# Kernel optimization log

Hardware: AMD Instinct MI355X
Metric: run time of the kernel (lower is better)

The kernel has to match this reference:

```python
import jax, jax.numpy as jnp
import numpy as np


def setup_inputs() -> dict:
    key = jax.random.key(0)
    k1, k2 = jax.random.split(key)
    B, C, H, W = 16, 128, 128, 128
    x = jax.random.normal(k1, (B, C, H, W), dtype=jnp.float32)
    # 1x1 conv weight, no bias: [out_channels, in_channels]
    w = jax.random.normal(k2, (C, C), dtype=jnp.float32) * (1.0 / np.sqrt(C))
    return {"x": x, "w": w}


def reference(x, w):
    # x: [B, C, H, W]; original computes y = x @ (x^T x) / (H*W) over flattened
    # spatial dim N = H*W, then a 1x1 conv. We reassociate exactly:
    #   x @ (x^T x) == (x x^T) @ x   (associativity of matmul)
    # avoiding the O(N^2) intermediate; math is identical.
    B, C, H, W = x.shape
    N = H * W
    xf = x.reshape(B, C, N)                              # [B, C, N]
    gram = jnp.einsum('bcn,bdn->bcd', xf, xf) / N        # [B, C, C] = (x x^T)/N
    y = jnp.einsum('bcd,bdn->bcn', gram, xf)             # [B, C, N]
    y = y.reshape(B, C, H, W)
    # 1x1 conv (bias=False) == per-pixel channel mixing
    out = jnp.einsum('oc,bchw->bohw', w, y)              # [B, C, H, W]
    return out
```

## Files before the change

kernel.cpp:

```cpp
#include <hip/hip_runtime.h>

typedef __attribute__((ext_vector_type(8))) short bf16x8;
typedef __attribute__((ext_vector_type(4))) float f32x4;
typedef __attribute__((ext_vector_type(4))) float f4v;
typedef __attribute__((ext_vector_type(4))) unsigned short u16x4;

#define NB 16
#define NC 128
#define NN 16384

__device__ __forceinline__ unsigned int f2bf_pack(float lo, float hi) {
  unsigned int ulo = __float_as_uint(lo);
  unsigned int uhi = __float_as_uint(hi);
  ulo = (ulo + 0x7FFFu + ((ulo >> 16) & 1u)) >> 16;
  uhi = (uhi + 0x7FFFu + ((uhi >> 16) & 1u)) & 0xFFFF0000u;
  return ulo | uhi;
}

__device__ __forceinline__ unsigned short f2bf_one(float v) {
  unsigned int u = __float_as_uint(v);
  return (unsigned short)((u + 0x7FFFu + ((u >> 16) & 1u)) >> 16);
}

__device__ __forceinline__ float bf2f(unsigned short u) {
  return __uint_as_float(((unsigned int)u) << 16);
}

__global__ __launch_bounds__(256, 2)
void nlm_gram_kernel(const float* __restrict__ x, unsigned short* __restrict__ partials,
                     int chunks, int ksteps) {
  __shared__ __align__(16) char lds[2 * 128 * 64 * 2];
  const int t = threadIdx.x;
  const int b  = blockIdx.x / chunks;
  const int ch = blockIdx.x % chunks;
  const int lane = t & 63, wv = t >> 6, l15 = lane & 15, q = lane >> 4;
  const int kc = ksteps * 64;

  const float* xb = x + (size_t)b * NC * NN + (size_t)ch * kc;

  f32x4 acc[2][8];
#pragma unroll
  for (int i = 0; i < 2; ++i)
#pragma unroll
    for (int j = 0; j < 8; ++j) acc[i][j] = (f32x4){0.f, 0.f, 0.f, 0.f};

  int srow[4], sseg[4];
#pragma unroll
  for (int i = 0; i < 4; ++i) { int id = t + 256 * i; srow[i] = id >> 3; sseg[i] = id & 7; }

  f4v pfA[4][2], pfB[4][2];

#define LOADPF(PF, KS)                                                      \
  {                                                                         \
    _Pragma("unroll") for (int i = 0; i < 4; ++i) {                         \
      const float* src = xb + (size_t)srow[i] * NN + (KS)*64 + sseg[i] * 8; \
      PF[i][0] = *(const f4v*)src;                                          \
      PF[i][1] = *(const f4v*)(src + 4);                                    \
    }                                                                       \
  }

#define PACKPF(PF, BUF)                                                     \
  {                                                                         \
    _Pragma("unroll") for (int i = 0; i < 4; ++i) {                         \
      uint4 pk;                                                             \
      pk.x = f2bf_pack(PF[i][0][0], PF[i][0][1]);                           \
      pk.y = f2bf_pack(PF[i][0][2], PF[i][0][3]);                           \
      pk.z = f2bf_pack(PF[i][1][0], PF[i][1][1]);                           \
      pk.w = f2bf_pack(PF[i][1][2], PF[i][1][3]);                           \
      int byte = (srow[i] * 128 + sseg[i] * 16) ^ ((srow[i] & 7) << 4);     \
      *(uint4*)((BUF) + byte) = pk;                                         \
    }                                                                       \
  }

#define MFMAPH(BUF)                                                                          \
  {                                                                                          \
    _Pragma("unroll") for (int kh = 0; kh < 2; ++kh) {                                       \
      const int kbyte = kh * 64 + q * 16;                                                    \
      int ra = wv * 32 + l15;                                                                \
      bf16x8 a0 = *(const bf16x8*)((BUF) + ((ra * 128 + kbyte) ^ ((ra & 7) << 4)));          \
      int rb = wv * 32 + 16 + l15;                                                           \
      bf16x8 a1 = *(const bf16x8*)((BUF) + ((rb * 128 + kbyte) ^ ((rb & 7) << 4)));          \
      _Pragma("unroll") for (int ct = 0; ct < 8; ++ct) {                                     \
        int rc = ct * 16 + l15;                                                              \
        bf16x8 bb = *(const bf16x8*)((BUF) + ((rc * 128 + kbyte) ^ ((rc & 7) << 4)));        \
        acc[0][ct] = __builtin_amdgcn_mfma_f32_16x16x32_bf16(a0, bb, acc[0][ct], 0, 0, 0);   \
        acc[1][ct] = __builtin_amdgcn_mfma_f32_16x16x32_bf16(a1, bb, acc[1][ct], 0, 0, 0);   \
      }                                                                                      \
    }                                                                                        \
  }

  char* buf0 = lds;
  char* buf1 = lds + 16384;

  LOADPF(pfA, 0);
  PACKPF(pfA, buf0);
  if (1 < ksteps) LOADPF(pfB, 1);
  __syncthreads();

  for (int ks = 0; ks < ksteps; ks += 2) {
    if (ks + 2 < ksteps) LOADPF(pfA, ks + 2);
    MFMAPH(buf0);
    if (ks + 1 < ksteps) PACKPF(pfB, buf1);
    __syncthreads();
    if (ks + 1 < ksteps) {
      if (ks + 3 < ksteps) LOADPF(pfB, ks + 3);
      MFMAPH(buf1);
      if (ks + 2 < ksteps) PACKPF(pfA, buf0);
      __syncthreads();
    }
  }

  unsigned short* part = partials + (size_t)blockIdx.x * (NC * NC);
#pragma unroll
  for (int rt = 0; rt < 2; ++rt)
#pragma unroll
    for (int ct = 0; ct < 8; ++ct)
#pragma unroll
      for (int r = 0; r < 4; ++r) {
        int i = wv * 32 + rt * 16 + q * 4 + r;
        int j = ct * 16 + l15;
        part[i * 128 + j] = f2bf_one(acc[rt][ct][r]);
      }
#undef LOADPF
#undef PACKPF
#undef MFMAPH
}

__global__ __launch_bounds__(256)
void nlm_gramw_kernel(const unsigned short* __restrict__ partials, const float* __restrict__ w,
                      unsigned short* __restrict__ Mbf, int chunks) {
  __shared__ __align__(16) float glds[8 * 128];
  const int t = threadIdx.x;
  const int b  = blockIdx.x >> 4;
  const int d0 = (blockIdx.x & 15) * 8;

  const int rr = t >> 5;
  const int c4 = (t & 31) * 4;
  const unsigned short* pb =
      partials + (size_t)b * chunks * (NC * NC) + (d0 + rr) * 128 + c4;
  f4v s = (f4v){0.f, 0.f, 0.f, 0.f};
  for (int chn = 0; chn < chunks; ++chn) {
    u16x4 v = *(const u16x4*)(pb + (size_t)chn * (NC * NC));
    s[0] += bf2f(v[0]);
    s[1] += bf2f(v[1]);
    s[2] += bf2f(v[2]);
    s[3] += bf2f(v[3]);
  }
  s *= (1.0f / 16384.0f);
  *(f4v*)(glds + rr * 128 + c4) = s;
  __syncthreads();

  const int o  = t & 127;
  const int j0 = (t >> 7) * 4;
  float m[4] = {0.f, 0.f, 0.f, 0.f};
  for (int c = 0; c < 128; c += 4) {
    f4v wv = *(const f4v*)(w + o * 128 + c);
#pragma unroll
    for (int j = 0; j < 4; ++j) {
      f4v gv = *(const f4v*)(glds + (j0 + j) * 128 + c);
      m[j] = fmaf(wv[0], gv[0], m[j]);
      m[j] = fmaf(wv[1], gv[1], m[j]);
      m[j] = fmaf(wv[2], gv[2], m[j]);
      m[j] = fmaf(wv[3], gv[3], m[j]);
    }
  }
  uint2 pk;
  pk.x = f2bf_pack(m[0], m[1]);
  pk.y = f2bf_pack(m[2], m[3]);
  *(uint2*)(Mbf + (size_t)b * NC * NC + o * 128 + d0 + j0) = pk;
}

__global__ __launch_bounds__(256, 2)
void nlm_out_kernel(const float* __restrict__ x, const unsigned short* __restrict__ Mbf,
                    float* __restrict__ out) {
  __shared__ __align__(16) char lds[128 * 128 * 2];
  const int t = threadIdx.x;
  const int b = (NB - 1) - (blockIdx.x >> 7);
  const int n0 = (blockIdx.x & 127) * 128;
  const int lane = t & 63, wv = t >> 6, l15 = lane & 15, q = lane >> 4;

  bf16x8 afr[2][4];
  const unsigned short* mb = Mbf + (size_t)b * NC * NC;
#pragma unroll
  for (int rt = 0; rt < 2; ++rt)
#pragma unroll
    for (int ks = 0; ks < 4; ++ks) {
      int o = wv * 32 + rt * 16 + l15;
      afr[rt][ks] = *(const bf16x8*)(mb + o * 128 + ks * 32 + q * 8);
    }

  const float* xb = x + (size_t)b * NC * NN + n0;
#pragma unroll
  for (int i = 0; i < 2; ++i) {
    int id = t + 256 * i;
    int nb = id & 31, cb = id >> 5;
    const float* src = xb + (size_t)(cb * 8) * NN + nb * 4;
    f4v v[8];
#pragma unroll
    for (int r = 0; r < 8; ++r) v[r] = *(const f4v*)(src + (size_t)r * NN);
#pragma unroll
    for (int j = 0; j < 4; ++j) {
      int n = nb * 4 + j;
      uint4 pk;
      pk.x = f2bf_pack(v[0][j], v[1][j]);
      pk.y = f2bf_pack(v[2][j], v[3][j]);
      pk.z = f2bf_pack(v[4][j], v[5][j]);
      pk.w = f2bf_pack(v[6][j], v[7][j]);
      int byte = (n * 256 + cb * 16) ^ ((((n & 7) ^ ((n >> 3) & 7))) << 4);
      *(uint4*)(lds + byte) = pk;
    }
  }
  __syncthreads();

  f32x4 acc[2][8];
#pragma unroll
  for (int i = 0; i < 2; ++i)
#pragma unroll
    for (int j = 0; j < 8; ++j) acc[i][j] = (f32x4){0.f, 0.f, 0.f, 0.f};

#pragma unroll
  for (int ks = 0; ks < 4; ++ks) {
#pragma unroll
    for (int ct = 0; ct < 8; ++ct) {
      int n = ct * 16 + l15;
      int byte = (n * 256 + ks * 64 + q * 16) ^ ((((n & 7) ^ ((n >> 3) & 7))) << 4);
      bf16x8 bfr = *(const bf16x8*)(lds + byte);
      acc[0][ct] = __builtin_amdgcn_mfma_f32_16x16x32_bf16(afr[0][ks], bfr, acc[0][ct], 0, 0, 0);
      acc[1][ct] = __builtin_amdgcn_mfma_f32_16x16x32_bf16(afr[1][ks], bfr, acc[1][ct], 0, 0, 0);
    }
  }

  float* ob = out + (size_t)b * NC * NN + n0;
#pragma unroll
  for (int rt = 0; rt < 2; ++rt)
#pragma unroll
    for (int ct = 0; ct < 8; ++ct)
#pragma unroll
      for (int r = 0; r < 4; ++r) {
        int o = wv * 32 + rt * 16 + q * 4 + r;
        int n = ct * 16 + l15;
        ob[(size_t)o * NN + n] = acc[rt][ct][r];
      }
}

extern "C" void kernel_launch(void* const* d_in, const int* in_sizes, int n_in,
                              void* d_out, int out_size, void* d_ws, size_t ws_size,
                              hipStream_t stream) {
  const float* x = (const float*)d_in[0];
  const float* w = (const float*)d_in[1];
  float* out = (float*)d_out;

  int chunks = 32;
  while (chunks > 1 &&
         (size_t)NB * chunks * NC * NC * 2 +
         (size_t)NB * NC * NC * 2 > ws_size)
    chunks >>= 1;
  int ksteps = (NN / chunks) / 64;

  char* wsp = (char*)d_ws;
  unsigned short* partials = (unsigned short*)wsp;
  wsp += (size_t)NB * chunks * NC * NC * 2;
  unsigned short* Mbf = (unsigned short*)wsp;

  hipLaunchKernelGGL(nlm_gram_kernel, dim3(NB * chunks), dim3(256), 0, stream,
                     x, partials, chunks, ksteps);
  hipLaunchKernelGGL(nlm_gramw_kernel, dim3(NB * 16), dim3(256), 0, stream,
                     partials, w, Mbf, chunks);
  hipLaunchKernelGGL(nlm_out_kernel, dim3(NB * 128), dim3(256), 0, stream,
                     x, Mbf, out);
}
```

Baseline: 88.26 us.

## Fuse gram, weight-mix and output stages into one cooperative persistent kernel

Merges the three launches into a single cooperative kernel that runs the gram partials, the reduction with the 1x1 weight, and the output GEMM as phases separated by grid-wide syncs. The grid is sized to two blocks per CU, chunk count is derived from it, and each block then handles a contiguous range of output tiles while reusing its loaded M fragments. The goal is to remove launch gaps and the tail effects between kernels. The cost is two grid barriers and less flexible load balancing, and it falls back to the three-kernel path if the cooperative launch fails.

After: 235.5 us. 167% more time.

```diff
diff --git a/kernel.cpp b/kernel.cpp
--- a/kernel.cpp
+++ b/kernel.cpp
@@ -1,4 +1,7 @@
 #include <hip/hip_runtime.h>
+#include <hip/hip_cooperative_groups.h>
+
+namespace cg = cooperative_groups;
 
 typedef __attribute__((ext_vector_type(8))) short bf16x8;
 typedef __attribute__((ext_vector_type(4))) float f32x4;
@@ -22,33 +25,10 @@
   return (unsigned short)((u + 0x7FFFu + ((u >> 16) & 1u)) >> 16);
 }
 
-__device__ __forceinline__ float bf2f(unsigned short u) {
-  return __uint_as_float(((unsigned int)u) << 16);
-}
-
-__global__ __launch_bounds__(256, 2)
-void nlm_gram_kernel(const float* __restrict__ x, unsigned short* __restrict__ partials,
-                     int chunks, int ksteps) {
-  __shared__ __align__(16) char lds[2 * 128 * 64 * 2];
-  const int t = threadIdx.x;
-  const int b  = blockIdx.x / chunks;
-  const int ch = blockIdx.x % chunks;
-  const int lane = t & 63, wv = t >> 6, l15 = lane & 15, q = lane >> 4;
-  const int kc = ksteps * 64;
-
-  const float* xb = x + (size_t)b * NC * NN + (size_t)ch * kc;
-
-  f32x4 acc[2][8];
-#pragma unroll
-  for (int i = 0; i < 2; ++i)
-#pragma unroll
-    for (int j = 0; j < 8; ++j) acc[i][j] = (f32x4){0.f, 0.f, 0.f, 0.f};
-
-  int srow[4], sseg[4];
-#pragma unroll
-  for (int i = 0; i < 4; ++i) { int id = t + 256 * i; srow[i] = id >> 3; sseg[i] = id & 7; }
-
-  f4v pfA[4][2], pfB[4][2];
+__device__ __forceinline__ float bf2f(unsigned int u16) {
+  return __uint_as_float(u16 << 16);
+}
+
 
 #define LOADPF(PF, KS)                                                      \
   {                                                                         \
@@ -89,6 +69,26 @@
     }                                                                                        \
   }
 
+__device__ __forceinline__ void phaseA_body(const float* __restrict__ x,
+                                            unsigned short* __restrict__ partials,
+                                            char* lds, int t, int g, int chunks, int ksteps) {
+  const int b  = g / chunks;
+  const int ch = g % chunks;
+  const int lane = t & 63, wv = t >> 6, l15 = lane & 15, q = lane >> 4;
+  const int kc = ksteps * 64;
+  const float* xb = x + (size_t)b * NC * NN + (size_t)ch * kc;
+
+  f32x4 acc[2][8];
+#pragma unroll
+  for (int i = 0; i < 2; ++i)
+#pragma unroll
+    for (int j = 0; j < 8; ++j) acc[i][j] = (f32x4){0.f, 0.f, 0.f, 0.f};
+
+  int srow[4], sseg[4];
+#pragma unroll
+  for (int i = 0; i < 4; ++i) { int id = t + 256 * i; srow[i] = id >> 3; sseg[i] = id & 7; }
+
+  f4v pfA[4][2], pfB[4][2];
   char* buf0 = lds;
   char* buf1 = lds + 16384;
 
@@ -110,7 +110,7 @@
     }
   }
 
-  unsigned short* part = partials + (size_t)blockIdx.x * (NC * NC);
+  unsigned short* part = partials + (size_t)g * (NC * NC);
 #pragma unroll
   for (int rt = 0; rt < 2; ++rt)
 #pragma unroll
@@ -121,75 +121,54 @@
         int j = ct * 16 + l15;
         part[i * 128 + j] = f2bf_one(acc[rt][ct][r]);
       }
-#undef LOADPF
-#undef PACKPF
-#undef MFMAPH
-}
-
-__global__ __launch_bounds__(256)
-void nlm_gramw_kernel(const unsigned short* __restrict__ partials, const float* __restrict__ w,
-                      unsigned short* __restrict__ Mbf, int chunks) {
-  __shared__ __align__(16) float glds[8 * 128];
-  const int t = threadIdx.x;
-  const int b  = blockIdx.x >> 4;
-  const int d0 = (blockIdx.x & 15) * 8;
-
-  const int rr = t >> 5;
-  const int c4 = (t & 31) * 4;
+}
+
+__device__ __forceinline__ void phaseB_unit(const unsigned short* __restrict__ partials,
+                                            const float* __restrict__ w,
+                                            unsigned short* __restrict__ Mbf,
+                                            float* glds, int t, int u, int chunks) {
+  const int b  = u >> 5;
+  const int d0 = (u & 31) * 4;
+
+  const int rr = t >> 6;
+  const int c2 = (t & 63) * 2;
   const unsigned short* pb =
-      partials + (size_t)b * chunks * (NC * NC) + (d0 + rr) * 128 + c4;
-  f4v s = (f4v){0.f, 0.f, 0.f, 0.f};
+      partials + (size_t)b * chunks * (NC * NC) + (d0 + rr) * 128 + c2;
+  float s0 = 0.f, s1 = 0.f;
   for (int chn = 0; chn < chunks; ++chn) {
-    u16x4 v = *(const u16x4*)(pb + (size_t)chn * (NC * NC));
-    s[0] += bf2f(v[0]);
-    s[1] += bf2f(v[1]);
-    s[2] += bf2f(v[2]);
-    s[3] += bf2f(v[3]);
-  }
-  s *= (1.0f / 16384.0f);
-  *(f4v*)(glds + rr * 128 + c4) = s;
+    unsigned int v = *(const unsigned int*)(pb + (size_t)chn * (NC * NC));
+    s0 += bf2f(v & 0xFFFFu);
+    s1 += bf2f(v >> 16);
+  }
+  s0 *= (1.0f / 16384.0f);
+  s1 *= (1.0f / 16384.0f);
+  glds[rr * 128 + c2] = s0;
+  glds[rr * 128 + c2 + 1] = s1;
   __syncthreads();
 
   const int o  = t & 127;
-  const int j0 = (t >> 7) * 4;
-  float m[4] = {0.f, 0.f, 0.f, 0.f};
+  const int j0 = (t >> 7) * 2;
+  float m0 = 0.f, m1 = 0.f;
   for (int c = 0; c < 128; c += 4) {
-    f4v wv = *(const f4v*)(w + o * 128 + c);
-#pragma unroll
-    for (int j = 0; j < 4; ++j) {
-      f4v gv = *(const f4v*)(glds + (j0 + j) * 128 + c);
-      m[j] = fmaf(wv[0], gv[0], m[j]);
-      m[j] = fmaf(wv[1], gv[1], m[j]);
-      m[j] = fmaf(wv[2], gv[2], m[j]);
-      m[j] = fmaf(wv[3], gv[3], m[j]);
-    }
-  }
-  uint2 pk;
-  pk.x = f2bf_pack(m[0], m[1]);
-  pk.y = f2bf_pack(m[2], m[3]);
-  *(uint2*)(Mbf + (size_t)b * NC * NC + o * 128 + d0 + j0) = pk;
-}
-
-__global__ __launch_bounds__(256, 2)
-void nlm_out_kernel(const float* __restrict__ x, const unsigned short* __restrict__ Mbf,
-                    float* __restrict__ out) {
-  __shared__ __align__(16) char lds[128 * 128 * 2];
-  const int t = threadIdx.x;
-  const int b = (NB - 1) - (blockIdx.x >> 7);
-  const int n0 = (blockIdx.x & 127) * 128;
+    f4v wr = *(const f4v*)(w + o * 128 + c);
+    f4v ga = *(const f4v*)(glds + (j0 + 0) * 128 + c);
+    f4v gb = *(const f4v*)(glds + (j0 + 1) * 128 + c);
+    m0 = fmaf(wr[0], ga[0], m0); m0 = fmaf(wr[1], ga[1], m0);
+    m0 = fmaf(wr[2], ga[2], m0); m0 = fmaf(wr[3], ga[3], m0);
+    m1 = fmaf(wr[0], gb[0], m1); m1 = fmaf(wr[1], gb[1], m1);
+    m1 = fmaf(wr[2], gb[2], m1); m1 = fmaf(wr[3], gb[3], m1);
+  }
+  *(unsigned int*)(Mbf + (size_t)b * NC * NC + o * 128 + d0 + j0) = f2bf_pack(m0, m1);
+  __syncthreads();
+}
+
+__device__ __forceinline__ void phaseC_tile(const float* __restrict__ x,
+                                            const bf16x8 afr[2][4],
+                                            float* __restrict__ out,
+                                            char* lds, int t, int b, int n0) {
   const int lane = t & 63, wv = t >> 6, l15 = lane & 15, q = lane >> 4;
-
-  bf16x8 afr[2][4];
-  const unsigned short* mb = Mbf + (size_t)b * NC * NC;
-#pragma unroll
-  for (int rt = 0; rt < 2; ++rt)
-#pragma unroll
-    for (int ks = 0; ks < 4; ++ks) {
-      int o = wv * 32 + rt * 16 + l15;
-      afr[rt][ks] = *(const bf16x8*)(mb + o * 128 + ks * 32 + q * 8);
-    }
-
   const float* xb = x + (size_t)b * NC * NN + n0;
+
 #pragma unroll
   for (int i = 0; i < 2; ++i) {
     int id = t + 256 * i;
@@ -241,6 +220,79 @@
         int n = ct * 16 + l15;
         ob[(size_t)o * NN + n] = acc[rt][ct][r];
       }
+  __syncthreads();
+}
+
+__device__ __forceinline__ void loadM(const unsigned short* __restrict__ Mbf,
+                                      bf16x8 afr[2][4], int t, int b) {
+  const int lane = t & 63, wv = t >> 6, l15 = lane & 15, q = lane >> 4;
+  const unsigned short* mb = Mbf + (size_t)b * NC * NC;
+#pragma unroll
+  for (int rt = 0; rt < 2; ++rt)
+#pragma unroll
+    for (int ks = 0; ks < 4; ++ks) {
+      int o = wv * 32 + rt * 16 + l15;
+      afr[rt][ks] = *(const bf16x8*)(mb + o * 128 + ks * 32 + q * 8);
+    }
+}
+
+__global__ __launch_bounds__(256, 2)
+void nlm_fused_kernel(const float* __restrict__ x, const float* __restrict__ w,
+                      float* __restrict__ out, unsigned short* __restrict__ partials,
+                      unsigned short* __restrict__ Mbf, int chunks, int ksteps) {
+  __shared__ __align__(16) char lds[32768];
+  const int t = threadIdx.x;
+  const int g = blockIdx.x;
+  cg::grid_group grid = cg::this_grid();
+
+  phaseA_body(x, partials, lds, t, g, chunks, ksteps);
+
+  __threadfence();
+  grid.sync();
+
+  for (int u = g; u < NB * 32; u += gridDim.x)
+    phaseB_unit(partials, w, Mbf, (float*)lds, t, u, chunks);
+
+  __threadfence();
+  grid.sync();
+
+  {
+    const int tiles_per = (NB * 128) / gridDim.x;
+    const int tile0 = g * tiles_per;
+    const int b = tile0 >> 7;
+    bf16x8 afr[2][4];
+    loadM(Mbf, afr, t, b);
+    for (int it = 0; it < tiles_per; ++it) {
+      const int tile = tile0 + it;
+      phaseC_tile(x, afr, out, lds, t, b, (tile & 127) * 128);
+    }
+  }
+}
+
+__global__ __launch_bounds__(256, 2)
+void nlm_gram_kernel(const float* __restrict__ x, unsigned short* __restrict__ partials,
+                     int chunks, int ksteps) {
+  __shared__ __align__(16) char lds[32768];
+  phaseA_body(x, partials, lds, threadIdx.x, blockIdx.x, chunks, ksteps);
+}
+
+__global__ __launch_bounds__(256)
+void nlm_gramw_kernel(const unsigned short* __restrict__ partials, const float* __restrict__ w,
+                      unsigned short* __restrict__ Mbf, int chunks) {
+  __shared__ __align__(16) float glds[4 * 128];
+  phaseB_unit(partials, w, Mbf, glds, threadIdx.x, blockIdx.x, chunks);
+}
+
+__global__ __launch_bounds__(256, 2)
+void nlm_out_kernel(const float* __restrict__ x, const unsigned short* __restrict__ Mbf,
+                    float* __restrict__ out) {
+  __shared__ __align__(16) char lds[32768];
+  const int t = threadIdx.x;
+  const int b = blockIdx.x >> 7;
+  const int n0 = (blockIdx.x & 127) * 128;
+  bf16x8 afr[2][4];
+  loadM(Mbf, afr, t, b);
+  phaseC_tile(x, afr, out, lds, t, b, n0);
 }
 
 extern "C" void kernel_launch(void* const* d_in, const int* in_sizes, int n_in,
@@ -250,11 +302,17 @@
   const float* w = (const float*)d_in[1];
   float* out = (float*)d_out;
 
-  int chunks = 32;
-  while (chunks > 1 &&
-         (size_t)NB * chunks * NC * NC * 2 +
-         (size_t)NB * NC * NC * 2 > ws_size)
+  int maxB = 0;
+  (void)hipOccupancyMaxActiveBlocksPerMultiprocessor(
+      &maxB, (const void*)nlm_fused_kernel, 256, 0);
+  int blocksPerCU = (maxB >= 2) ? 2 : 1;
+  int coopGrid = blocksPerCU * 256;
+  int chunks = coopGrid / NB;
+  while (chunks > 16 &&
+         (size_t)NB * chunks * NC * NC * 2 + (size_t)NB * NC * NC * 2 > ws_size) {
     chunks >>= 1;
+    coopGrid = chunks * NB;
+  }
   int ksteps = (NN / chunks) / 64;
 
   char* wsp = (char*)d_ws;
@@ -262,10 +320,16 @@
   wsp += (size_t)NB * chunks * NC * NC * 2;
   unsigned short* Mbf = (unsigned short*)wsp;
 
-  hipLaunchKernelGGL(nlm_gram_kernel, dim3(NB * chunks), dim3(256), 0, stream,
-                     x, partials, chunks, ksteps);
-  hipLaunchKernelGGL(nlm_gramw_kernel, dim3(NB * 16), dim3(256), 0, stream,
-                     partials, w, Mbf, chunks);
-  hipLaunchKernelGGL(nlm_out_kernel, dim3(NB * 128), dim3(256), 0, stream,
-                     x, Mbf, out);
-}
+  void* kargs[] = {(void*)&x, (void*)&w, (void*)&out,
+                   (void*)&partials, (void*)&Mbf, (void*)&chunks, (void*)&ksteps};
+  hipError_t err = hipLaunchCooperativeKernel((const void*)nlm_fused_kernel,
+                                              dim3(coopGrid), dim3(256), kargs, 0, stream);
+  if (err != hipSuccess) {
+    hipLaunchKernelGGL(nlm_gram_kernel, dim3(NB * chunks), dim3(256), 0, stream,
+                       x, partials, chunks, ksteps);
+    hipLaunchKernelGGL(nlm_gramw_kernel, dim3(NB * 32), dim3(256), 0, stream,
+                       partials, w, Mbf, chunks);
+    hipLaunchKernelGGL(nlm_out_kernel, dim3(NB * 128), dim3(256), 0, stream,
+                       x, Mbf, out);
+  }
+}
```
